# Kernel tuning notes

Measured on AMD Instinct MI355X. Metric: run time of the kernel, lower is better.

Reference implementation:

```python
import jax, jax.numpy as jnp
import numpy as np

VOCAB = 32000
EMBED = 512
DEP_SIZE = 64
QKV = 512
B, S = 16, 1024
NEG = -1e10


def setup_inputs() -> dict:
    key = jax.random.key(0)
    ks = jax.random.split(key, 16)
    inputs = jax.random.randint(ks[0], (B, S), 0, VOCAB)
    dependency = jax.random.randint(ks[1], (B, S, S), 0, DEP_SIZE)
    embed_table = jax.random.normal(ks[2], (VOCAB, EMBED), dtype=jnp.float32) * 0.02
    dep_table = jax.random.normal(ks[3], (DEP_SIZE, 1), dtype=jnp.float32) * 0.02
    dep_table = dep_table.at[0].set(0.0)  # padding_idx=0
    sc = 1.0 / np.sqrt(EMBED)
    Wq = jax.random.normal(ks[4], (EMBED, QKV), dtype=jnp.float32) * sc
    bq = jnp.zeros((QKV,), jnp.float32)
    Wk = jax.random.normal(ks[5], (EMBED, QKV), dtype=jnp.float32) * sc
    bk = jnp.zeros((QKV,), jnp.float32)
    Wv = jax.random.normal(ks[6], (EMBED, QKV), dtype=jnp.float32) * sc
    bv = jnp.zeros((QKV,), jnp.float32)
    scv = 1.0 / np.sqrt(QKV)
    W1 = jax.random.normal(ks[7], (QKV, QKV), dtype=jnp.float32) * scv
    b1 = jnp.zeros((QKV,), jnp.float32)
    W2 = jax.random.normal(ks[8], (QKV, QKV), dtype=jnp.float32) * scv
    b2 = jnp.zeros((QKV,), jnp.float32)
    return dict(inputs=inputs, dependency=dependency, embed_table=embed_table,
                dep_table=dep_table, Wq=Wq, bq=bq, Wk=Wk, bk=bk, Wv=Wv, bv=bv,
                W1=W1, b1=b1, W2=W2, b2=b2)


def reference(inputs, dependency, embed_table, dep_table, Wq, bq, Wk, bk, Wv, bv, W1, b1, W2, b2):
    x = jnp.take(embed_table, inputs, axis=0)                  # [B,S,E]
    dep_emb = jnp.take(dep_table, dependency, axis=0)[..., 0]  # [B,S,S]
    q = x @ Wq + bq                                            # [B,S,D]
    k = x @ Wk + bk
    v = x @ Wv + bv
    attn = jnp.einsum('bqd,bkd->bqk', q, k) * dep_emb          # [B,S,S]
    attn = jnp.where(dependency == 0, NEG, attn)
    weights = jax.nn.softmax(attn, axis=-1)
    wm = jnp.einsum('bqk,bkd->bqd', weights, v)                # fused weighted sum
    wm = jnp.tanh(wm @ W1 + b1) @ W2 + b2
    return wm, weights
```

## Files before the change

### kernel.cpp

```cpp
#include <hip/hip_runtime.h>

typedef __attribute__((ext_vector_type(8))) short short8;
typedef __attribute__((ext_vector_type(4))) float floatx4;

__device__ __forceinline__ unsigned short f2b(float f) {
  unsigned int u = __float_as_uint(f);
  unsigned int r = (u + 0x7FFFu + ((u >> 16) & 1u)) >> 16;
  return (unsigned short)r;
}
__device__ __forceinline__ uint4 ld8f(const float* p) {
  float4 a = *(const float4*)p;
  float4 b = *(const float4*)(p + 4);
  uint4 r;
  r.x = (unsigned int)f2b(a.x) | ((unsigned int)f2b(a.y) << 16);
  r.y = (unsigned int)f2b(a.z) | ((unsigned int)f2b(a.w) << 16);
  r.z = (unsigned int)f2b(b.x) | ((unsigned int)f2b(b.y) << 16);
  r.w = (unsigned int)f2b(b.z) | ((unsigned int)f2b(b.w) << 16);
  return r;
}

__device__ __forceinline__ void xcd_swz(int& bx, int& by, int& bz) {
  const int nx = gridDim.x, ny = gridDim.y;
  const int nwg = nx * ny * gridDim.z;
  const int lbid = blockIdx.x + nx * (blockIdx.y + ny * blockIdx.z);
  const int s = (lbid & 7) * (nwg >> 3) + (lbid >> 3);
  bx = s % nx; by = (s / nx) % ny; bz = s / (nx * ny);
}

__device__ __forceinline__ void kloop(const unsigned short* __restrict__ A,
                                      const unsigned short* __restrict__ B,
                                      int K, unsigned short* ldsA, unsigned short* ldsB,
                                      floatx4 (&acc)[2][4])
{
  const int tid = threadIdx.x;
  const int w = tid >> 6, lane = tid & 63;
  const int quad = lane >> 4, l16 = lane & 15;
  const int wy = w >> 1, wx = w & 1;
  const int rsa = 16 * w + (lane >> 2);
  const int rsb = 32 * w + (lane >> 2);
  const int ks = (lane & 3) * 8;
  const int loa  = w * 512 + lane * 8;
  const int lob0 = w * 1024 + lane * 8;
  const int lob1 = lob0 + 512;
  const unsigned short* ga  = A + (size_t)rsa * K + ks;
  const unsigned short* gb0 = B + (size_t)rsb * K + ks;
  const unsigned short* gb1 = gb0 + (size_t)16 * K;
  const int NT = K >> 5;

  uint4 va  = *(const uint4*)ga;
  uint4 vb0 = *(const uint4*)gb0;
  uint4 vb1 = *(const uint4*)gb1;
  *(uint4*)&ldsA[loa]  = va;
  *(uint4*)&ldsB[lob0] = vb0;
  *(uint4*)&ldsB[lob1] = vb1;
  asm volatile("s_waitcnt lgkmcnt(0)" ::: "memory");
  __builtin_amdgcn_s_barrier();
  __builtin_amdgcn_sched_barrier(0);

  int p = 0;
  for (int t = 0; t < NT; ++t) {
    if (t + 1 < NT) {
      const int k0 = (t + 1) * 32;
      va  = *(const uint4*)(ga + k0);
      vb0 = *(const uint4*)(gb0 + k0);
      vb1 = *(const uint4*)(gb1 + k0);
    }
    const int cb = p ? 2048 : 0, cbB = p ? 4096 : 0;
    short8 af[2], bf[4];
#pragma unroll
    for (int i = 0; i < 2; i++)
      af[i] = *(const short8*)&ldsA[cb + (wy * 32 + i * 16 + l16) * 32 + quad * 8];
#pragma unroll
    for (int j = 0; j < 4; j++)
      bf[j] = *(const short8*)&ldsB[cbB + (wx * 64 + j * 16 + l16) * 32 + quad * 8];
#pragma unroll
    for (int i = 0; i < 2; i++)
#pragma unroll
      for (int j = 0; j < 4; j++)
        acc[i][j] = __builtin_amdgcn_mfma_f32_16x16x32_bf16(af[i], bf[j], acc[i][j], 0, 0, 0);
    if (t + 1 < NT) {
      const int nb = p ? 0 : 2048, nbB = p ? 0 : 4096;
      *(uint4*)&ldsA[nb + loa]   = va;
      *(uint4*)&ldsB[nbB + lob0] = vb0;
      *(uint4*)&ldsB[nbB + lob1] = vb1;
    }
    asm volatile("s_waitcnt lgkmcnt(0)" ::: "memory");
    __builtin_amdgcn_s_barrier();
    __builtin_amdgcn_sched_barrier(0);
    p ^= 1;
  }
}

__global__ __launch_bounds__(256, 3) void gemm_qkv(
    const unsigned short* __restrict__ x,
    const unsigned short* __restrict__ WT,
    const float* __restrict__ bq, const float* __restrict__ bk, const float* __restrict__ bv,
    unsigned short* __restrict__ q, unsigned short* __restrict__ kx, unsigned short* __restrict__ v)
{
  __shared__ unsigned short ldsA[4096], ldsB[8192];
  int bx, by, bz;
  xcd_swz(bx, by, bz);
  const int m0 = by * 64, n0 = bx * 128;
  floatx4 acc[2][4];
#pragma unroll
  for (int i = 0; i < 2; i++)
#pragma unroll
    for (int j = 0; j < 4; j++) acc[i][j] = (floatx4){0.f, 0.f, 0.f, 0.f};

  kloop(x + (size_t)m0 * 512, WT + (size_t)n0 * 512, 512, ldsA, ldsB, acc);

  const int seg = n0 >> 9, nloc = n0 & 511;
  unsigned short* C = seg == 0 ? q : (seg == 1 ? kx : v);
  const float* bias = seg == 0 ? bq : (seg == 1 ? bk : bv);
  const int lane = threadIdx.x & 63, w = threadIdx.x >> 6;
  const int quad = lane >> 4, l16 = lane & 15, wy = w >> 1, wx = w & 1;
  float bvv[4];
#pragma unroll
  for (int j = 0; j < 4; j++) bvv[j] = bias[nloc + wx * 64 + j * 16 + l16];
#pragma unroll
  for (int i = 0; i < 2; i++)
#pragma unroll
    for (int r = 0; r < 4; r++) {
      int m = m0 + wy * 32 + i * 16 + quad * 4 + r;
      unsigned short* crow = C + (size_t)m * 512 + nloc + wx * 64 + l16;
#pragma unroll
      for (int j = 0; j < 4; j++) crow[j * 16] = f2b(acc[i][j][r] + bvv[j]);
    }
}

template<int CF32, int ACT>
__global__ __launch_bounds__(256, 3) void gemm2(
    const unsigned short* __restrict__ A, const unsigned short* __restrict__ Bt,
    const float* __restrict__ bias, void* __restrict__ Cv,
    int N, int K, long aB, long bB, long cB)
{
  __shared__ unsigned short ldsA[4096], ldsB[8192];
  int bx, by, bz;
  xcd_swz(bx, by, bz);
  const int b = bz;
  const int m0 = by * 64, n0 = bx * 128;
  floatx4 acc[2][4];
#pragma unroll
  for (int i = 0; i < 2; i++)
#pragma unroll
    for (int j = 0; j < 4; j++) acc[i][j] = (floatx4){0.f, 0.f, 0.f, 0.f};

  kloop(A + (size_t)b * aB + (size_t)m0 * K, Bt + (size_t)b * bB + (size_t)n0 * K,
        K, ldsA, ldsB, acc);

  const int lane = threadIdx.x & 63, w = threadIdx.x >> 6;
  const int quad = lane >> 4, l16 = lane & 15, wy = w >> 1, wx = w & 1;
  float bvv[4];
#pragma unroll
  for (int j = 0; j < 4; j++)
    bvv[j] = bias ? bias[n0 + wx * 64 + j * 16 + l16] : 0.f;
  float*          Cf = (float*)Cv          + (size_t)b * cB;
  unsigned short* Ch = (unsigned short*)Cv + (size_t)b * cB;
#pragma unroll
  for (int i = 0; i < 2; i++)
#pragma unroll
    for (int r = 0; r < 4; r++) {
      int m = m0 + wy * 32 + i * 16 + quad * 4 + r;
      size_t base = (size_t)m * N + n0 + wx * 64 + l16;
#pragma unroll
      for (int j = 0; j < 4; j++) {
        float vv = acc[i][j][r] + bvv[j];
        if (ACT == 1) vv = tanhf(vv);
        if (CF32) Cf[base + j * 16] = vv;
        else      Ch[base + j * 16] = f2b(vv);
      }
    }
}

#define CST 132
__global__ __launch_bounds__(256, 3) void score_kernel(
    const unsigned short* __restrict__ Q, const unsigned short* __restrict__ Km,
    const int* __restrict__ dep, const float* __restrict__ dept,
    float* __restrict__ E)
{
  __shared__ union {
    struct { unsigned short a[4096]; unsigned short b[8192]; } s;
    float c[32 * CST];
  } sm;
  __shared__ float dtab[64];
  const int tid = threadIdx.x;
  if (tid < 64) dtab[tid] = dept[tid];

  int bx, by, bz;
  xcd_swz(bx, by, bz);
  const int b = bz;
  const int m0 = by * 64, n0 = bx * 128;
  floatx4 acc[2][4];
#pragma unroll
  for (int i = 0; i < 2; i++)
#pragma unroll
    for (int j = 0; j < 4; j++) acc[i][j] = (floatx4){0.f, 0.f, 0.f, 0.f};

  kloop(Q + (size_t)b * (1024 * 512) + (size_t)m0 * 512,
        Km + (size_t)b * (1024 * 512) + (size_t)n0 * 512,
        512, sm.s.a, sm.s.b, acc);

  const int lane = tid & 63, w = tid >> 6;
  const int quad = lane >> 4, l16 = lane & 15, wy = w >> 1, wx = w & 1;
  const int* depb = dep + (size_t)b * 1024 * 1024;
  float* Eb = E + (size_t)b * 1024 * 1024;
  const int cr = tid >> 3, cb = (tid & 7) * 16;

#pragma unroll
  for (int i = 0; i < 2; i++) {
    __syncthreads();
#pragma unroll
    for (int j = 0; j < 4; j++)
#pragma unroll
      for (int r = 0; r < 4; r++)
        sm.c[(wy * 16 + quad * 4 + r) * CST + wx * 64 + j * 16 + l16] = acc[i][j][r];
    __syncthreads();
    const int m = m0 + (cr >> 4) * 32 + i * 16 + (cr & 15);
    const int* dr = depb + (size_t)m * 1024 + n0 + cb;
    float* er = Eb + (size_t)m * 1024 + n0 + cb;
    const float* crow = &sm.c[cr * CST + cb];
#pragma unroll
    for (int c = 0; c < 4; c++) {
      int4 d = *(const int4*)(dr + c * 4);
      float4 s = *(const float4*)(crow + c * 4);
      float4 e;
      e.x = d.x ? __expf(fminf(fmaxf(s.x * dtab[d.x & 63], -60.f), 60.f)) : 0.f;
      e.y = d.y ? __expf(fminf(fmaxf(s.y * dtab[d.y & 63], -60.f), 60.f)) : 0.f;
      e.z = d.z ? __expf(fminf(fmaxf(s.z * dtab[d.z & 63], -60.f), 60.f)) : 0.f;
      e.w = d.w ? __expf(fminf(fmaxf(s.w * dtab[d.w & 63], -60.f), 60.f)) : 0.f;
      *(float4*)(er + c * 4) = e;
    }
  }
}

__global__ void build_x(const float* __restrict__ embed, const int* __restrict__ inputs,
                        unsigned short* __restrict__ x)
{
  const int row = blockIdx.x * 4 + (threadIdx.x >> 6);
  const int lane = threadIdx.x & 63;
  const float* src = embed + (size_t)inputs[row] * 512 + lane * 8;
  *(uint4*)&x[(size_t)row * 512 + lane * 8] = ld8f(src);
}

__global__ void trans_w(const float* s0, const float* s1, const float* s2,
                        const float* s3, const float* s4, unsigned short* dst)
{
  __shared__ unsigned short tile[32][33];
  const int z = blockIdx.z;
  const float* src = z == 0 ? s0 : z == 1 ? s1 : z == 2 ? s2 : z == 3 ? s3 : s4;
  unsigned short* ob = dst + (size_t)z * 262144;
  int c0 = blockIdx.x * 32, r0 = blockIdx.y * 32;
  int tx = threadIdx.x & 31, ty = threadIdx.x >> 5;
  for (int i = ty; i < 32; i += 8)
    tile[i][tx] = f2b(src[(size_t)(r0 + i) * 512 + (c0 + tx)]);
  __syncthreads();
  for (int i = ty; i < 32; i += 8)
    ob[(size_t)(c0 + i) * 512 + (r0 + tx)] = tile[tx][i];
}

__global__ void trans_v(const unsigned short* __restrict__ in, unsigned short* __restrict__ out)
{
  __shared__ unsigned short tile[32][33];
  const unsigned short* ib = in + (size_t)blockIdx.z * (1024 * 512);
  unsigned short* ob = out + (size_t)blockIdx.z * (512 * 1024);
  int c0 = blockIdx.x * 32, r0 = blockIdx.y * 32;
  int tx = threadIdx.x & 31, ty = threadIdx.x >> 5;
  for (int i = ty; i < 32; i += 8)
    tile[i][tx] = ib[(size_t)(r0 + i) * 512 + (c0 + tx)];
  __syncthreads();
  for (int i = ty; i < 32; i += 8)
    ob[(size_t)(c0 + i) * 1024 + (r0 + tx)] = tile[tx][i];
}

__global__ void normalize_rows(float* __restrict__ wf, unsigned short* __restrict__ wb)
{
  size_t row = blockIdx.x;
  float4* p = (float4*)(wf + row * 1024);
  float4 u = p[threadIdx.x];
  float s = (u.x + u.y) + (u.z + u.w);
#pragma unroll
  for (int d = 1; d < 64; d <<= 1) s += __shfl_xor(s, d);
  __shared__ float acc4[4];
  if ((threadIdx.x & 63) == 0) acc4[threadIdx.x >> 6] = s;
  __syncthreads();
  float tot = (acc4[0] + acc4[1]) + (acc4[2] + acc4[3]);
  float inv = tot > 0.f ? 1.f / tot : 0.f;
  u.x *= inv; u.y *= inv; u.z *= inv; u.w *= inv;
  p[threadIdx.x] = u;
  uint2 pk;
  pk.x = (unsigned int)f2b(u.x) | ((unsigned int)f2b(u.y) << 16);
  pk.y = (unsigned int)f2b(u.z) | ((unsigned int)f2b(u.w) << 16);
  *(uint2*)&wb[row * 1024 + threadIdx.x * 4] = pk;
}

extern "C" void kernel_launch(void* const* d_in, const int* in_sizes, int n_in,
                              void* d_out, int out_size, void* d_ws, size_t ws_size,
                              hipStream_t stream)
{
  const int*   inputs     = (const int*)d_in[0];
  const int*   dependency = (const int*)d_in[1];
  const float* embed      = (const float*)d_in[2];
  const float* dept       = (const float*)d_in[3];
  const float* Wq = (const float*)d_in[4];   const float* bq = (const float*)d_in[5];
  const float* Wk = (const float*)d_in[6];   const float* bk = (const float*)d_in[7];
  const float* Wv = (const float*)d_in[8];   const float* bvv = (const float*)d_in[9];
  const float* W1 = (const float*)d_in[10];  const float* b1 = (const float*)d_in[11];
  const float* W2 = (const float*)d_in[12];  const float* b2 = (const float*)d_in[13];

  float* out  = (float*)d_out;
  float* wout = out + (size_t)8388608;

  unsigned short* ws   = (unsigned short*)d_ws;
  unsigned short* q    = ws;
  unsigned short* kx   = ws + 8388608;
  unsigned short* WTc  = ws + 16777216;
  unsigned short* W1T  = ws + 17563648;
  unsigned short* W2T  = ws + 17825792;
  unsigned short* wbf  = ws;
  unsigned short* h    = ws;

  unsigned short* x    = (unsigned short*)wout;
  unsigned short* v    = (unsigned short*)out;
  unsigned short* vT   = (unsigned short*)out + 8388608;
  unsigned short* wmp  = (unsigned short*)out;

  dim3 blk(256);

  trans_w<<<dim3(16, 16, 5), blk, 0, stream>>>(Wq, Wk, Wv, W1, W2, WTc);
  build_x<<<dim3(4096), blk, 0, stream>>>(embed, inputs, x);

  gemm_qkv<<<dim3(12, 256, 1), blk, 0, stream>>>(x, WTc, bq, bk, bvv, q, kx, v);

  score_kernel<<<dim3(8, 16, 16), blk, 0, stream>>>(q, kx, dependency, dept, wout);

  trans_v<<<dim3(16, 32, 16), blk, 0, stream>>>(v, vT);

  normalize_rows<<<dim3(16384), blk, 0, stream>>>(wout, wbf);

  gemm2<0, 0><<<dim3(4, 16, 16), blk, 0, stream>>>(wbf, vT, nullptr, wmp,
                                                   512, 1024, 1024L * 1024, 512L * 1024, 1024L * 512);
  gemm2<0, 1><<<dim3(4, 256, 1), blk, 0, stream>>>(wmp, W1T, b1, h, 512, 512, 0, 0, 0);
  gemm2<1, 0><<<dim3(4, 256, 1), blk, 0, stream>>>(h, W2T, b2, out, 512, 512, 0, 0, 0);
}
```

Measured before the change: 397.2 us.

## Fuse embedding gather into QKV GEMM and widen K-tile to 64

Removes the separate build_x kernel by gathering embedding rows (fp32, converted to bf16 on the fly) directly inside the QKV GEMM's A-tile load. The shared K-loop now stages 64-wide K tiles instead of 32, halving the number of barriers per GEMM and doubling LDS per block. XCD swizzle now only remaps x/y within each z-slice for batched kernels. The larger LDS footprint may reduce occupancy, and the fp32 gather re-reads embedding rows once per N-tile, 12 times in total.

Measured after the change: 438.7 us. 10.4% more time.

```diff
diff --git a/kernel.cpp b/kernel.cpp
--- a/kernel.cpp
+++ b/kernel.cpp
@@ -8,51 +8,62 @@
   unsigned int r = (u + 0x7FFFu + ((u >> 16) & 1u)) >> 16;
   return (unsigned short)r;
 }
-__device__ __forceinline__ uint4 ld8f(const float* p) {
-  float4 a = *(const float4*)p;
-  float4 b = *(const float4*)(p + 4);
+__device__ __forceinline__ unsigned int pk2(float a, float b) {
+  return (unsigned int)f2b(a) | ((unsigned int)f2b(b) << 16);
+}
+__device__ __forceinline__ uint4 pack8(float4 a, float4 b) {
   uint4 r;
-  r.x = (unsigned int)f2b(a.x) | ((unsigned int)f2b(a.y) << 16);
-  r.y = (unsigned int)f2b(a.z) | ((unsigned int)f2b(a.w) << 16);
-  r.z = (unsigned int)f2b(b.x) | ((unsigned int)f2b(b.y) << 16);
-  r.w = (unsigned int)f2b(b.z) | ((unsigned int)f2b(b.w) << 16);
+  r.x = pk2(a.x, a.y); r.y = pk2(a.z, a.w);
+  r.z = pk2(b.x, b.y); r.w = pk2(b.z, b.w);
   return r;
 }
 
-__device__ __forceinline__ void xcd_swz(int& bx, int& by, int& bz) {
+__device__ __forceinline__ void xcd_swz2(int& bx, int& by) {
   const int nx = gridDim.x, ny = gridDim.y;
-  const int nwg = nx * ny * gridDim.z;
-  const int lbid = blockIdx.x + nx * (blockIdx.y + ny * blockIdx.z);
+  const int nwg = nx * ny;
+  const int lbid = blockIdx.x + nx * blockIdx.y;
   const int s = (lbid & 7) * (nwg >> 3) + (lbid >> 3);
-  bx = s % nx; by = (s / nx) % ny; bz = s / (nx * ny);
-}
-
-__device__ __forceinline__ void kloop(const unsigned short* __restrict__ A,
-                                      const unsigned short* __restrict__ B,
-                                      int K, unsigned short* ldsA, unsigned short* ldsB,
-                                      floatx4 (&acc)[2][4])
+  bx = s % nx; by = s / nx;
+}
+
+template<bool EMB>
+__device__ __forceinline__ void kloop64(const unsigned short* __restrict__ A,
+                                        const float* __restrict__ emb,
+                                        const int* __restrict__ inpRow,
+                                        const unsigned short* __restrict__ B,
+                                        int K, unsigned short* ldsA, unsigned short* ldsB,
+                                        floatx4 (&acc)[2][4])
 {
   const int tid = threadIdx.x;
   const int w = tid >> 6, lane = tid & 63;
   const int quad = lane >> 4, l16 = lane & 15;
   const int wy = w >> 1, wx = w & 1;
-  const int rsa = 16 * w + (lane >> 2);
-  const int rsb = 32 * w + (lane >> 2);
-  const int ks = (lane & 3) * 8;
-  const int loa  = w * 512 + lane * 8;
-  const int lob0 = w * 1024 + lane * 8;
-  const int lob1 = lob0 + 512;
-  const unsigned short* ga  = A + (size_t)rsa * K + ks;
-  const unsigned short* gb0 = B + (size_t)rsb * K + ks;
-  const unsigned short* gb1 = gb0 + (size_t)16 * K;
-  const int NT = K >> 5;
-
-  uint4 va  = *(const uint4*)ga;
-  uint4 vb0 = *(const uint4*)gb0;
-  uint4 vb1 = *(const uint4*)gb1;
-  *(uint4*)&ldsA[loa]  = va;
-  *(uint4*)&ldsB[lob0] = vb0;
-  *(uint4*)&ldsB[lob1] = vb1;
+  const int row = tid >> 2;
+  const int kc = (tid & 3) * 8;
+  const int loa  = row * 64 + kc;
+  const int lob0 = row * 64 + kc;
+  const int lob1 = lob0 + 4096;
+  const unsigned short* ga  = A + (size_t)row * K + kc;
+  const float*          gaf = EMB ? emb + (size_t)inpRow[row] * 512 + kc : nullptr;
+  const unsigned short* gb0 = B + (size_t)row * K + kc;
+  const unsigned short* gb1 = gb0 + (size_t)64 * K;
+  const int NT = K >> 6;
+
+  uint4 va0, va1, vb00, vb01, vb10, vb11;
+  float4 fa0, fa1, fa2, fa3;
+
+  if (EMB) {
+    fa0 = *(const float4*)(gaf);      fa1 = *(const float4*)(gaf + 4);
+    fa2 = *(const float4*)(gaf + 32); fa3 = *(const float4*)(gaf + 36);
+    va0 = pack8(fa0, fa1); va1 = pack8(fa2, fa3);
+  } else {
+    va0 = *(const uint4*)ga; va1 = *(const uint4*)(ga + 32);
+  }
+  vb00 = *(const uint4*)gb0; vb01 = *(const uint4*)(gb0 + 32);
+  vb10 = *(const uint4*)gb1; vb11 = *(const uint4*)(gb1 + 32);
+  *(uint4*)&ldsA[loa] = va0;       *(uint4*)&ldsA[loa + 32] = va1;
+  *(uint4*)&ldsB[lob0] = vb00;     *(uint4*)&ldsB[lob0 + 32] = vb01;
+  *(uint4*)&ldsB[lob1] = vb10;     *(uint4*)&ldsB[lob1 + 32] = vb11;
   asm volatile("s_waitcnt lgkmcnt(0)" ::: "memory");
   __builtin_amdgcn_s_barrier();
   __builtin_amdgcn_sched_barrier(0);
@@ -60,29 +71,40 @@
   int p = 0;
   for (int t = 0; t < NT; ++t) {
     if (t + 1 < NT) {
-      const int k0 = (t + 1) * 32;
-      va  = *(const uint4*)(ga + k0);
-      vb0 = *(const uint4*)(gb0 + k0);
-      vb1 = *(const uint4*)(gb1 + k0);
-    }
-    const int cb = p ? 2048 : 0, cbB = p ? 4096 : 0;
-    short8 af[2], bf[4];
-#pragma unroll
-    for (int i = 0; i < 2; i++)
-      af[i] = *(const short8*)&ldsA[cb + (wy * 32 + i * 16 + l16) * 32 + quad * 8];
-#pragma unroll
-    for (int j = 0; j < 4; j++)
-      bf[j] = *(const short8*)&ldsB[cbB + (wx * 64 + j * 16 + l16) * 32 + quad * 8];
-#pragma unroll
-    for (int i = 0; i < 2; i++)
+      const int k0 = (t + 1) * 64;
+      if (EMB) {
+        fa0 = *(const float4*)(gaf + k0);      fa1 = *(const float4*)(gaf + k0 + 4);
+        fa2 = *(const float4*)(gaf + k0 + 32); fa3 = *(const float4*)(gaf + k0 + 36);
+      } else {
+        va0 = *(const uint4*)(ga + k0); va1 = *(const uint4*)(ga + k0 + 32);
+      }
+      vb00 = *(const uint4*)(gb0 + k0); vb01 = *(const uint4*)(gb0 + k0 + 32);
+      vb10 = *(const uint4*)(gb1 + k0); vb11 = *(const uint4*)(gb1 + k0 + 32);
+    }
+    const int ca = p ? 4096 : 0, cb = p ? 8192 : 0;
+    short8 af[2][2], bf[2][4];
+#pragma unroll
+    for (int s = 0; s < 2; s++) {
+#pragma unroll
+      for (int i = 0; i < 2; i++)
+        af[s][i] = *(const short8*)&ldsA[ca + (wy * 32 + i * 16 + l16) * 64 + s * 32 + quad * 8];
 #pragma unroll
       for (int j = 0; j < 4; j++)
-        acc[i][j] = __builtin_amdgcn_mfma_f32_16x16x32_bf16(af[i], bf[j], acc[i][j], 0, 0, 0);
+        bf[s][j] = *(const short8*)&ldsB[cb + (wx * 64 + j * 16 + l16) * 64 + s * 32 + quad * 8];
+    }
+#pragma unroll
+    for (int s = 0; s < 2; s++)
+#pragma unroll
+      for (int i = 0; i < 2; i++)
+#pragma unroll
+        for (int j = 0; j < 4; j++)
+          acc[i][j] = __builtin_amdgcn_mfma_f32_16x16x32_bf16(af[s][i], bf[s][j], acc[i][j], 0, 0, 0);
     if (t + 1 < NT) {
-      const int nb = p ? 0 : 2048, nbB = p ? 0 : 4096;
-      *(uint4*)&ldsA[nb + loa]   = va;
-      *(uint4*)&ldsB[nbB + lob0] = vb0;
-      *(uint4*)&ldsB[nbB + lob1] = vb1;
+      const int na = p ? 0 : 4096, nb = p ? 0 : 8192;
+      if (EMB) { va0 = pack8(fa0, fa1); va1 = pack8(fa2, fa3); }
+      *(uint4*)&ldsA[na + loa] = va0;    *(uint4*)&ldsA[na + loa + 32] = va1;
+      *(uint4*)&ldsB[nb + lob0] = vb00;  *(uint4*)&ldsB[nb + lob0 + 32] = vb01;
+      *(uint4*)&ldsB[nb + lob1] = vb10;  *(uint4*)&ldsB[nb + lob1 + 32] = vb11;
     }
     asm volatile("s_waitcnt lgkmcnt(0)" ::: "memory");
     __builtin_amdgcn_s_barrier();
@@ -92,14 +114,15 @@
 }
 
 __global__ __launch_bounds__(256, 3) void gemm_qkv(
-    const unsigned short* __restrict__ x,
+    const float* __restrict__ embed,
+    const int* __restrict__ inputs,
     const unsigned short* __restrict__ WT,
     const float* __restrict__ bq, const float* __restrict__ bk, const float* __restrict__ bv,
     unsigned short* __restrict__ q, unsigned short* __restrict__ kx, unsigned short* __restrict__ v)
 {
-  __shared__ unsigned short ldsA[4096], ldsB[8192];
-  int bx, by, bz;
-  xcd_swz(bx, by, bz);
+  __shared__ unsigned short ldsA[8192], ldsB[16384];
+  int bx, by;
+  xcd_swz2(bx, by);
   const int m0 = by * 64, n0 = bx * 128;
   floatx4 acc[2][4];
 #pragma unroll
@@ -107,7 +130,7 @@
 #pragma unroll
     for (int j = 0; j < 4; j++) acc[i][j] = (floatx4){0.f, 0.f, 0.f, 0.f};
 
-  kloop(x + (size_t)m0 * 512, WT + (size_t)n0 * 512, 512, ldsA, ldsB, acc);
+  kloop64<true>(nullptr, embed, inputs + m0, WT + (size_t)n0 * 512, 512, ldsA, ldsB, acc);
 
   const int seg = n0 >> 9, nloc = n0 & 511;
   unsigned short* C = seg == 0 ? q : (seg == 1 ? kx : v);
@@ -134,10 +157,10 @@
     const float* __restrict__ bias, void* __restrict__ Cv,
     int N, int K, long aB, long bB, long cB)
 {
-  __shared__ unsigned short ldsA[4096], ldsB[8192];
-  int bx, by, bz;
-  xcd_swz(bx, by, bz);
-  const int b = bz;
+  __shared__ unsigned short ldsA[8192], ldsB[16384];
+  int bx, by;
+  xcd_swz2(bx, by);
+  const int b = blockIdx.z;
   const int m0 = by * 64, n0 = bx * 128;
   floatx4 acc[2][4];
 #pragma unroll
@@ -145,8 +168,8 @@
 #pragma unroll
     for (int j = 0; j < 4; j++) acc[i][j] = (floatx4){0.f, 0.f, 0.f, 0.f};
 
-  kloop(A + (size_t)b * aB + (size_t)m0 * K, Bt + (size_t)b * bB + (size_t)n0 * K,
-        K, ldsA, ldsB, acc);
+  kloop64<false>(A + (size_t)b * aB + (size_t)m0 * K, nullptr, nullptr,
+                 Bt + (size_t)b * bB + (size_t)n0 * K, K, ldsA, ldsB, acc);
 
   const int lane = threadIdx.x & 63, w = threadIdx.x >> 6;
   const int quad = lane >> 4, l16 = lane & 15, wy = w >> 1, wx = w & 1;
@@ -179,16 +202,16 @@
     float* __restrict__ E)
 {
   __shared__ union {
-    struct { unsigned short a[4096]; unsigned short b[8192]; } s;
+    struct { unsigned short a[8192]; unsigned short b[16384]; } s;
     float c[32 * CST];
   } sm;
   __shared__ float dtab[64];
   const int tid = threadIdx.x;
   if (tid < 64) dtab[tid] = dept[tid];
 
-  int bx, by, bz;
-  xcd_swz(bx, by, bz);
-  const int b = bz;
+  int bx, by;
+  xcd_swz2(bx, by);
+  const int b = blockIdx.z;
   const int m0 = by * 64, n0 = bx * 128;
   floatx4 acc[2][4];
 #pragma unroll
@@ -196,9 +219,8 @@
 #pragma unroll
     for (int j = 0; j < 4; j++) acc[i][j] = (floatx4){0.f, 0.f, 0.f, 0.f};
 
-  kloop(Q + (size_t)b * (1024 * 512) + (size_t)m0 * 512,
-        Km + (size_t)b * (1024 * 512) + (size_t)n0 * 512,
-        512, sm.s.a, sm.s.b, acc);
+  kloop64<false>(Q + (size_t)b * (1024 * 512) + (size_t)m0 * 512, nullptr, nullptr,
+                 Km + (size_t)b * (1024 * 512) + (size_t)n0 * 512, 512, sm.s.a, sm.s.b, acc);
 
   const int lane = tid & 63, w = tid >> 6;
   const int quad = lane >> 4, l16 = lane & 15, wy = w >> 1, wx = w & 1;
@@ -231,15 +253,6 @@
       *(float4*)(er + c * 4) = e;
     }
   }
-}
-
-__global__ void build_x(const float* __restrict__ embed, const int* __restrict__ inputs,
-                        unsigned short* __restrict__ x)
-{
-  const int row = blockIdx.x * 4 + (threadIdx.x >> 6);
-  const int lane = threadIdx.x & 63;
-  const float* src = embed + (size_t)inputs[row] * 512 + lane * 8;
-  *(uint4*)&x[(size_t)row * 512 + lane * 8] = ld8f(src);
 }
 
 __global__ void trans_w(const float* s0, const float* s1, const float* s2,
@@ -288,8 +301,8 @@
   u.x *= inv; u.y *= inv; u.z *= inv; u.w *= inv;
   p[threadIdx.x] = u;
   uint2 pk;
-  pk.x = (unsigned int)f2b(u.x) | ((unsigned int)f2b(u.y) << 16);
-  pk.y = (unsigned int)f2b(u.z) | ((unsigned int)f2b(u.w) << 16);
+  pk.x = pk2(u.x, u.y);
+  pk.y = pk2(u.z, u.w);
   *(uint2*)&wb[row * 1024 + threadIdx.x * 4] = pk;
 }
 
@@ -319,7 +332,6 @@
   unsigned short* wbf  = ws;
   unsigned short* h    = ws;
 
-  unsigned short* x    = (unsigned short*)wout;
   unsigned short* v    = (unsigned short*)out;
   unsigned short* vT   = (unsigned short*)out + 8388608;
   unsigned short* wmp  = (unsigned short*)out;
@@ -327,9 +339,8 @@
   dim3 blk(256);
 
   trans_w<<<dim3(16, 16, 5), blk, 0, stream>>>(Wq, Wk, Wv, W1, W2, WTc);
-  build_x<<<dim3(4096), blk, 0, stream>>>(embed, inputs, x);
-
-  gemm_qkv<<<dim3(12, 256, 1), blk, 0, stream>>>(x, WTc, bq, bk, bvv, q, kx, v);
+
+  gemm_qkv<<<dim3(12, 256, 1), blk, 0, stream>>>(embed, inputs, WTc, bq, bk, bvv, q, kx, v);
 
   score_kernel<<<dim3(8, 16, 16), blk, 0, stream>>>(q, kx, dependency, dept, wout);
 
```
